# Optimization experiments

Hardware: AMD Instinct MI355X
Metric: run time of the kernel (lower is better)

The kernel has to match this reference:

```python
import jax, jax.numpy as jnp
import numpy as np

# Module hyper-params (match init_kwargs)
IN_C, OUT_C = 64, 64
KH, KW = 3, 3            # kernel_size_2d
UNIT = 16                # unit_size (width of virtual 2D feature map)
K = KH * KW              # equivalent 1D kernel size = 9
PAD = (K - 1) // 2       # = 4


def _tap_positions(T):
    # Fixed integer deform-conv offsets: tap j in group g = j // KW gets
    # x-offset (UNIT - KW) * (g - center_group).
    center = (KH - 1) // 2
    off = np.array([(UNIT - KW) * (j // KW - center) for j in range(K)], dtype=np.int32)
    # deform-conv sample position for output t, tap j (stride=1, dilation=1):
    #   pos = t - PAD + j + off[j]
    pos = np.arange(T, dtype=np.int32)[None, :] - PAD + np.arange(K, dtype=np.int32)[:, None] + off[:, None]  # [K, T]
    valid = (pos >= 0) & (pos < T)
    return np.clip(pos, 0, T - 1), valid


def setup_inputs() -> dict:
    key = jax.random.key(0)
    k1, k2, k3 = jax.random.split(key, 3)
    B, T = 8, 65536
    x = jax.random.normal(k1, (B, IN_C, T), dtype=jnp.float32)
    # weight init: uniform(-stdv, stdv), stdv = 1/sqrt(in_c * 1 * K)
    stdv = 1.0 / float(np.sqrt(IN_C * K))
    weight = jax.random.uniform(k2, (OUT_C, IN_C, K), jnp.float32, -stdv, stdv)
    # bias init: uniform(-bound, bound), bound = 1/sqrt(fan_in) = stdv
    bias = jax.random.uniform(k3, (OUT_C,), jnp.float32, -stdv, stdv)
    return {"x": x, "weight": weight, "bias": bias}


def reference(x, weight, bias):
    B, C, T = x.shape
    pos, valid = _tap_positions(T)
    pos = jnp.asarray(pos)
    valid = jnp.asarray(valid)
    # integer gather (offsets are integer so bilinear sampling is exact), zero outside
    xg = jnp.where(valid[None, None], x[:, :, pos], 0.0)  # [B, C, K, T]
    out = jnp.einsum('ock,bckt->bot', weight, xg)          # [B, OUT_C, T]
    return out + bias[None, :, None]
```

## Files before the change

### kernel.cpp

```cpp
#include <hip/hip_runtime.h>


typedef short bf16x8 __attribute__((ext_vector_type(8)));
typedef short bf16x4 __attribute__((ext_vector_type(4)));
typedef float f32x4  __attribute__((ext_vector_type(4)));

#define T_LEN   65536
#define NT      256
#define ROWS    296
#define PITCH   68
#define LOFF    20
#define NCHUNK  18
#define OPITCH  260
#define SMEM_BYTES (ROWS * PITCH * 2)

__device__ __forceinline__ short f2bf(float f) {
    union { float f; unsigned u; } v; v.f = f;
    unsigned u = v.u;
    u += 0x7fffu + ((u >> 16) & 1u);
    return (short)(u >> 16);
}

__global__ void prep_w_kernel(const float* __restrict__ w, short* __restrict__ W2) {
    int idx = blockIdx.x * 256 + threadIdx.x;
    if (idx >= 4 * NCHUNK * 64) return;
    int lane = idx & 63;
    int g    = idx >> 6;
    int ch   = g >> 2;
    int mt   = g & 3;
    int o    = mt * 16 + (lane & 15);
    bf16x8 v;
#pragma unroll
    for (int i = 0; i < 8; ++i) {
        int kk = ch * 32 + (lane >> 4) * 8 + i;
        int j = kk >> 6, c = kk & 63;
        v[i] = f2bf(w[o * 576 + c * 9 + j]);
    }
    *(bf16x8*)(W2 + (size_t)idx * 8) = v;
}

__global__ __launch_bounds__(256, 3)
void ta_main_kernel(const float* __restrict__ x, const short* __restrict__ W2,
                    const float* __restrict__ bias, float* __restrict__ out) {
    __shared__ __align__(16) char smem[SMEM_BYTES];
    short* xs = (short*)smem;
    float* os = (float*)smem;

    const int tid  = threadIdx.x;
    const int wv   = tid >> 6;
    const int lane = tid & 63;
    const int l15  = lane & 15;
    const int quad = lane >> 4;
    const int b    = blockIdx.y;
    const int bxd  = blockIdx.x;
    const int bx   = (bxd & 7) * 32 + (bxd >> 3);
    const int t0   = bx * NT;

    const int c = tid >> 2;
    const int q = tid & 3;
    const float* xrow = x + (((size_t)(b * 64 + c)) << 16);
    const int tbase = t0 - LOFF;
    const bool interior = (t0 >= LOFF) && (t0 + (ROWS - LOFF) <= T_LEN);

    if (interior) {
        f32x4 v[19];
#pragma unroll
        for (int i = 0; i < 19; ++i) {
            const int f = q + 4 * i;
            if (f < 74) v[i] = *(const f32x4*)(xrow + tbase + 4 * f);
        }
#pragma unroll
        for (int i = 0; i < 19; ++i) {
            const int f = q + 4 * i;
            if (f < 74) {
                const int tt = 4 * f;
                xs[(tt + 0) * PITCH + c] = f2bf(v[i][0]);
                xs[(tt + 1) * PITCH + c] = f2bf(v[i][1]);
                xs[(tt + 2) * PITCH + c] = f2bf(v[i][2]);
                xs[(tt + 3) * PITCH + c] = f2bf(v[i][3]);
            }
        }
    } else {
#pragma unroll
        for (int i = 0; i < 19; ++i) {
            const int f = q + 4 * i;
            if (f < 74) {
                const int tt = 4 * f;
                const int tg = tbase + tt;
                f32x4 v;
                v[0] = ((unsigned)(tg + 0) < (unsigned)T_LEN) ? xrow[tg + 0] : 0.f;
                v[1] = ((unsigned)(tg + 1) < (unsigned)T_LEN) ? xrow[tg + 1] : 0.f;
                v[2] = ((unsigned)(tg + 2) < (unsigned)T_LEN) ? xrow[tg + 2] : 0.f;
                v[3] = ((unsigned)(tg + 3) < (unsigned)T_LEN) ? xrow[tg + 3] : 0.f;
                xs[(tt + 0) * PITCH + c] = f2bf(v[0]);
                xs[(tt + 1) * PITCH + c] = f2bf(v[1]);
                xs[(tt + 2) * PITCH + c] = f2bf(v[2]);
                xs[(tt + 3) * PITCH + c] = f2bf(v[3]);
            }
        }
    }
    __syncthreads();

    int bbase[4];
#pragma unroll
    for (int nt = 0; nt < 4; ++nt) {
        const int tl = wv * 64 + nt * 16 + l15;
        bbase[nt] = (tl + 3) * PITCH + quad * 8;
    }
    const short* w2p = W2 + (size_t)lane * 8;

    f32x4 acc[4][4] = {};

    const int dtab[9] = {-17, -16, -15, -1, 0, 1, 15, 16, 17};

    bf16x8 a_cur[4], b_cur[4], a_nxt[4], b_nxt[4];

    {
        const int roff0 = (dtab[0] + 17) * PITCH + 0;
#pragma unroll
        for (int mt = 0; mt < 4; ++mt)
            a_cur[mt] = *(const bf16x8*)(w2p + (size_t)(0 * 4 + mt) * 512);
#pragma unroll
        for (int nt = 0; nt < 4; ++nt) {
            union { bf16x8 v8; bf16x4 v4[2]; } u;
            u.v4[0] = *(const bf16x4*)(xs + bbase[nt] + roff0);
            u.v4[1] = *(const bf16x4*)(xs + bbase[nt] + roff0 + 4);
            b_cur[nt] = u.v8;
        }
    }

#pragma unroll
    for (int ch = 0; ch < NCHUNK; ++ch) {
        if (ch < NCHUNK - 1) {
            const int chn = ch + 1;
            const int jn = chn >> 1, hn = chn & 1;
            const int roffn = (dtab[jn] + 17) * PITCH + hn * 32;
#pragma unroll
            for (int mt = 0; mt < 4; ++mt)
                a_nxt[mt] = *(const bf16x8*)(w2p + (size_t)(chn * 4 + mt) * 512);
#pragma unroll
            for (int nt = 0; nt < 4; ++nt) {
                union { bf16x8 v8; bf16x4 v4[2]; } u;
                u.v4[0] = *(const bf16x4*)(xs + bbase[nt] + roffn);
                u.v4[1] = *(const bf16x4*)(xs + bbase[nt] + roffn + 4);
                b_nxt[nt] = u.v8;
            }
        }
#pragma unroll
        for (int mt = 0; mt < 4; ++mt)
#pragma unroll
            for (int nt = 0; nt < 4; ++nt)
                acc[mt][nt] = __builtin_amdgcn_mfma_f32_16x16x32_bf16(a_cur[mt], b_cur[nt], acc[mt][nt], 0, 0, 0);
        if (ch < NCHUNK - 1) {
#pragma unroll
            for (int mt = 0; mt < 4; ++mt) { a_cur[mt] = a_nxt[mt]; b_cur[mt] = b_nxt[mt]; }
        }
    }

    const size_t outb = ((size_t)(b * 64)) << 16;
#pragma unroll
    for (int p = 0; p < 2; ++p) {
        __syncthreads();
#pragma unroll
        for (int mtl = 0; mtl < 2; ++mtl) {
            const int mt = 2 * p + mtl;
#pragma unroll
            for (int r = 0; r < 4; ++r) {
                const int ol = mtl * 16 + quad * 4 + r;
                const float bv = bias[mt * 16 + quad * 4 + r];
#pragma unroll
                for (int nt = 0; nt < 4; ++nt) {
                    const int t = wv * 64 + nt * 16 + l15;
                    os[ol * OPITCH + t] = acc[mt][nt][r] + bv;
                }
            }
        }
        __syncthreads();
#pragma unroll
        for (int i = 0; i < 8; ++i) {
            const int item = tid + 256 * i;
            const int ol = item >> 6;
            const int f4 = item & 63;
            const f32x4 v = *(const f32x4*)(os + ol * OPITCH + 4 * f4);
            const int o = p * 32 + ol;
            *(f32x4*)(out + outb + (((size_t)o) << 16) + t0 + 4 * f4) = v;
        }
    }
}

extern "C" void kernel_launch(void* const* d_in, const int* in_sizes, int n_in,
                              void* d_out, int out_size, void* d_ws, size_t ws_size,
                              hipStream_t stream) {
    const float* x    = (const float*)d_in[0];
    const float* w    = (const float*)d_in[1];
    const float* bias = (const float*)d_in[2];
    float* out = (float*)d_out;
    short* W2  = (short*)d_ws;

    hipLaunchKernelGGL(prep_w_kernel, dim3(18), dim3(256), 0, stream, w, W2);
    hipLaunchKernelGGL(ta_main_kernel, dim3(T_LEN / NT, 8), dim3(256), 0, stream,
                       x, W2, bias, out);
}
```

Before: 286.7 us.

## Make blocks persistent over four time tiles with prefetched next-tile input

Each block now handles four consecutive 256-sample tiles instead of one. It issues global loads for the next tile into registers before the MFMA loop of the current tile, then writes them to LDS during the epilogue, once the input buffer is free. Input and output staging get separate shared buffers, and occupancy drops from 3 to 2 blocks per CU to leave room for the extra registers and LDS. The aim is to hide global load latency behind compute, at the cost of fewer resident waves and a smaller grid of 512 blocks.

```diff
diff --git a/kernel.cpp b/kernel.cpp
--- a/kernel.cpp
+++ b/kernel.cpp
@@ -7,12 +7,15 @@
 
 #define T_LEN   65536
 #define NT      256
+#define NTILE   4
+#define SPAN    (NT * NTILE)
 #define ROWS    296
 #define PITCH   68
 #define LOFF    20
 #define NCHUNK  18
 #define OPITCH  260
-#define SMEM_BYTES (ROWS * PITCH * 2)
+#define XS_SHORTS (ROWS * PITCH)
+#define OS_FLOATS (32 * OPITCH)
 
 __device__ __forceinline__ short f2bf(float f) {
     union { float f; unsigned u; } v; v.f = f;
@@ -39,12 +42,11 @@
     *(bf16x8*)(W2 + (size_t)idx * 8) = v;
 }
 
-__global__ __launch_bounds__(256, 3)
+__global__ __launch_bounds__(256, 2)
 void ta_main_kernel(const float* __restrict__ x, const short* __restrict__ W2,
                     const float* __restrict__ bias, float* __restrict__ out) {
-    __shared__ __align__(16) char smem[SMEM_BYTES];
-    short* xs = (short*)smem;
-    float* os = (float*)smem;
+    __shared__ __align__(16) short xs[XS_SHORTS];
+    __shared__ __align__(16) float os[OS_FLOATS];
 
     const int tid  = threadIdx.x;
     const int wv   = tid >> 6;
@@ -53,22 +55,41 @@
     const int quad = lane >> 4;
     const int b    = blockIdx.y;
     const int bxd  = blockIdx.x;
-    const int bx   = (bxd & 7) * 32 + (bxd >> 3);
-    const int t0   = bx * NT;
+    const int bx   = (bxd & 7) * 8 + (bxd >> 3);
+    const int tg0  = bx * SPAN;
 
     const int c = tid >> 2;
     const int q = tid & 3;
     const float* xrow = x + (((size_t)(b * 64 + c)) << 16);
-    const int tbase = t0 - LOFF;
-    const bool interior = (t0 >= LOFF) && (t0 + (ROWS - LOFF) <= T_LEN);
-
-    if (interior) {
-        f32x4 v[19];
-#pragma unroll
-        for (int i = 0; i < 19; ++i) {
-            const int f = q + 4 * i;
-            if (f < 74) v[i] = *(const f32x4*)(xrow + tbase + 4 * f);
-        }
+
+    f32x4 v[19];
+
+    auto issue = [&](const int t0) {
+        const int tbase = t0 - LOFF;
+        const bool interior = (t0 >= LOFF) && (t0 + (ROWS - LOFF) <= T_LEN);
+        if (interior) {
+#pragma unroll
+            for (int i = 0; i < 19; ++i) {
+                const int f = q + 4 * i;
+                if (f < 74) v[i] = *(const f32x4*)(xrow + tbase + 4 * f);
+            }
+        } else {
+#pragma unroll
+            for (int i = 0; i < 19; ++i) {
+                const int f = q + 4 * i;
+                if (f < 74) {
+                    const int tg = tbase + 4 * f;
+                    f32x4 t;
+                    t[0] = ((unsigned)(tg + 0) < (unsigned)T_LEN) ? xrow[tg + 0] : 0.f;
+                    t[1] = ((unsigned)(tg + 1) < (unsigned)T_LEN) ? xrow[tg + 1] : 0.f;
+                    t[2] = ((unsigned)(tg + 2) < (unsigned)T_LEN) ? xrow[tg + 2] : 0.f;
+                    t[3] = ((unsigned)(tg + 3) < (unsigned)T_LEN) ? xrow[tg + 3] : 0.f;
+                    v[i] = t;
+                }
+            }
+        }
+    };
+    auto commit = [&]() {
 #pragma unroll
         for (int i = 0; i < 19; ++i) {
             const int f = q + 4 * i;
@@ -80,25 +101,10 @@
                 xs[(tt + 3) * PITCH + c] = f2bf(v[i][3]);
             }
         }
-    } else {
-#pragma unroll
-        for (int i = 0; i < 19; ++i) {
-            const int f = q + 4 * i;
-            if (f < 74) {
-                const int tt = 4 * f;
-                const int tg = tbase + tt;
-                f32x4 v;
-                v[0] = ((unsigned)(tg + 0) < (unsigned)T_LEN) ? xrow[tg + 0] : 0.f;
-                v[1] = ((unsigned)(tg + 1) < (unsigned)T_LEN) ? xrow[tg + 1] : 0.f;
-                v[2] = ((unsigned)(tg + 2) < (unsigned)T_LEN) ? xrow[tg + 2] : 0.f;
-                v[3] = ((unsigned)(tg + 3) < (unsigned)T_LEN) ? xrow[tg + 3] : 0.f;
-                xs[(tt + 0) * PITCH + c] = f2bf(v[0]);
-                xs[(tt + 1) * PITCH + c] = f2bf(v[1]);
-                xs[(tt + 2) * PITCH + c] = f2bf(v[2]);
-                xs[(tt + 3) * PITCH + c] = f2bf(v[3]);
-            }
-        }
-    }
+    };
+
+    issue(tg0);
+    commit();
     __syncthreads();
 
     int bbase[4];
@@ -108,82 +114,87 @@
         bbase[nt] = (tl + 3) * PITCH + quad * 8;
     }
     const short* w2p = W2 + (size_t)lane * 8;
-
-    f32x4 acc[4][4] = {};
-
+    const size_t outb = ((size_t)(b * 64)) << 16;
     const int dtab[9] = {-17, -16, -15, -1, 0, 1, 15, 16, 17};
 
-    bf16x8 a_cur[4], b_cur[4], a_nxt[4], b_nxt[4];
-
-    {
-        const int roff0 = (dtab[0] + 17) * PITCH + 0;
-#pragma unroll
-        for (int mt = 0; mt < 4; ++mt)
-            a_cur[mt] = *(const bf16x8*)(w2p + (size_t)(0 * 4 + mt) * 512);
-#pragma unroll
-        for (int nt = 0; nt < 4; ++nt) {
-            union { bf16x8 v8; bf16x4 v4[2]; } u;
-            u.v4[0] = *(const bf16x4*)(xs + bbase[nt] + roff0);
-            u.v4[1] = *(const bf16x4*)(xs + bbase[nt] + roff0 + 4);
-            b_cur[nt] = u.v8;
-        }
-    }
-
-#pragma unroll
-    for (int ch = 0; ch < NCHUNK; ++ch) {
-        if (ch < NCHUNK - 1) {
-            const int chn = ch + 1;
-            const int jn = chn >> 1, hn = chn & 1;
-            const int roffn = (dtab[jn] + 17) * PITCH + hn * 32;
+    for (int it = 0; it < NTILE; ++it) {
+        const int t0 = tg0 + it * NT;
+        const bool more = (it + 1 < NTILE);
+
+        if (more) issue(t0 + NT);
+
+        f32x4 acc[4][4] = {};
+        bf16x8 a_cur[4], b_cur[4], a_nxt[4], b_nxt[4];
+        {
+            const int roff0 = (dtab[0] + 17) * PITCH + 0;
 #pragma unroll
             for (int mt = 0; mt < 4; ++mt)
-                a_nxt[mt] = *(const bf16x8*)(w2p + (size_t)(chn * 4 + mt) * 512);
+                a_cur[mt] = *(const bf16x8*)(w2p + (size_t)(0 * 4 + mt) * 512);
 #pragma unroll
             for (int nt = 0; nt < 4; ++nt) {
                 union { bf16x8 v8; bf16x4 v4[2]; } u;
-                u.v4[0] = *(const bf16x4*)(xs + bbase[nt] + roffn);
-                u.v4[1] = *(const bf16x4*)(xs + bbase[nt] + roffn + 4);
-                b_nxt[nt] = u.v8;
-            }
-        }
-#pragma unroll
-        for (int mt = 0; mt < 4; ++mt)
-#pragma unroll
-            for (int nt = 0; nt < 4; ++nt)
-                acc[mt][nt] = __builtin_amdgcn_mfma_f32_16x16x32_bf16(a_cur[mt], b_cur[nt], acc[mt][nt], 0, 0, 0);
-        if (ch < NCHUNK - 1) {
-#pragma unroll
-            for (int mt = 0; mt < 4; ++mt) { a_cur[mt] = a_nxt[mt]; b_cur[mt] = b_nxt[mt]; }
-        }
-    }
-
-    const size_t outb = ((size_t)(b * 64)) << 16;
-#pragma unroll
-    for (int p = 0; p < 2; ++p) {
+                u.v4[0] = *(const bf16x4*)(xs + bbase[nt] + roff0);
+                u.v4[1] = *(const bf16x4*)(xs + bbase[nt] + roff0 + 4);
+                b_cur[nt] = u.v8;
+            }
+        }
+#pragma unroll
+        for (int ch = 0; ch < NCHUNK; ++ch) {
+            if (ch < NCHUNK - 1) {
+                const int chn = ch + 1;
+                const int jn = chn >> 1, hn = chn & 1;
+                const int roffn = (dtab[jn] + 17) * PITCH + hn * 32;
+#pragma unroll
+                for (int mt = 0; mt < 4; ++mt)
+                    a_nxt[mt] = *(const bf16x8*)(w2p + (size_t)(chn * 4 + mt) * 512);
+#pragma unroll
+                for (int nt = 0; nt < 4; ++nt) {
+                    union { bf16x8 v8; bf16x4 v4[2]; } u;
+                    u.v4[0] = *(const bf16x4*)(xs + bbase[nt] + roffn);
+                    u.v4[1] = *(const bf16x4*)(xs + bbase[nt] + roffn + 4);
+                    b_nxt[nt] = u.v8;
+                }
+            }
+#pragma unroll
+            for (int mt = 0; mt < 4; ++mt)
+#pragma unroll
+                for (int nt = 0; nt < 4; ++nt)
+                    acc[mt][nt] = __builtin_amdgcn_mfma_f32_16x16x32_bf16(a_cur[mt], b_cur[nt], acc[mt][nt], 0, 0, 0);
+            if (ch < NCHUNK - 1) {
+#pragma unroll
+                for (int mt = 0; mt < 4; ++mt) { a_cur[mt] = a_nxt[mt]; b_cur[mt] = b_nxt[mt]; }
+            }
+        }
+
         __syncthreads();
 #pragma unroll
-        for (int mtl = 0; mtl < 2; ++mtl) {
-            const int mt = 2 * p + mtl;
-#pragma unroll
-            for (int r = 0; r < 4; ++r) {
-                const int ol = mtl * 16 + quad * 4 + r;
-                const float bv = bias[mt * 16 + quad * 4 + r];
-#pragma unroll
-                for (int nt = 0; nt < 4; ++nt) {
-                    const int t = wv * 64 + nt * 16 + l15;
-                    os[ol * OPITCH + t] = acc[mt][nt][r] + bv;
+        for (int p = 0; p < 2; ++p) {
+            if (p == 1) __syncthreads();
+#pragma unroll
+            for (int mtl = 0; mtl < 2; ++mtl) {
+                const int mt = 2 * p + mtl;
+#pragma unroll
+                for (int r = 0; r < 4; ++r) {
+                    const int ol = mtl * 16 + quad * 4 + r;
+                    const float bv = bias[mt * 16 + quad * 4 + r];
+#pragma unroll
+                    for (int nt = 0; nt < 4; ++nt) {
+                        const int t = wv * 64 + nt * 16 + l15;
+                        os[ol * OPITCH + t] = acc[mt][nt][r] + bv;
+                    }
                 }
             }
-        }
-        __syncthreads();
-#pragma unroll
-        for (int i = 0; i < 8; ++i) {
-            const int item = tid + 256 * i;
-            const int ol = item >> 6;
-            const int f4 = item & 63;
-            const f32x4 v = *(const f32x4*)(os + ol * OPITCH + 4 * f4);
-            const int o = p * 32 + ol;
-            *(f32x4*)(out + outb + (((size_t)o) << 16) + t0 + 4 * f4) = v;
+            if (p == 0 && more) commit();
+            __syncthreads();
+#pragma unroll
+            for (int i = 0; i < 8; ++i) {
+                const int item = tid + 256 * i;
+                const int ol = item >> 6;
+                const int f4 = item & 63;
+                const f32x4 vv = *(const f32x4*)(os + ol * OPITCH + 4 * f4);
+                const int o = p * 32 + ol;
+                *(f32x4*)(out + outb + (((size_t)o) << 16) + t0 + 4 * f4) = vv;
+            }
         }
     }
 }
@@ -198,6 +209,6 @@
     short* W2  = (short*)d_ws;
 
     hipLaunchKernelGGL(prep_w_kernel, dim3(18), dim3(256), 0, stream, w, W2);
-    hipLaunchKernelGGL(ta_main_kernel, dim3(T_LEN / NT, 8), dim3(256), 0, stream,
+    hipLaunchKernelGGL(ta_main_kernel, dim3(T_LEN / SPAN, 8), dim3(256), 0, stream,
                        x, W2, bias, out);
 }
```

Result: slower. 394.1 us (+37.5%).
